# Optimization experiments

Measured on AMD Instinct MI355X. Metric: run time of the kernel, lower is better.

Reference implementation:

```python
import jax, jax.numpy as jnp
import numpy as np

TOKEN_BITS = 10
CODEBOOK_SIZE = 2 ** TOKEN_BITS
COMMITMENT_COST = 0.25
ENT_WEIGHT = 0.1
ENT_TEMP = 0.01
ENT_GAMMA = 1.0
EPS = 1e-5


def _make_codebook():
    bits_to_indices = 2 ** np.arange(TOKEN_BITS, dtype=np.int64)  # [c]
    all_codes = np.arange(CODEBOOK_SIZE, dtype=np.int64)  # [n]
    bits = ((all_codes[:, None] & bits_to_indices) != 0).astype(np.float32)
    return jnp.asarray(bits * 2.0 - 1.0)  # [n, c] in {-1, +1}


def setup_inputs() -> dict:
    key = jax.random.key(0)
    z = jax.random.normal(key, (64, 10, 32, 32), dtype=jnp.float32)  # [b, c, h, w]
    codebook = _make_codebook()  # [1024, 10]
    return {"z": z, "codebook": codebook}


def reference(z, codebook):
    # b c h w -> b h w c
    zc = jnp.transpose(z, (0, 2, 3, 1))
    # strategy == 'default': sign quantization to {-1, +1}
    z_hard = jnp.where(zc > 0.0, 1.0, -1.0).astype(zc.dtype)

    # bit-pack indices (bits represented by sign)
    bits_to_indices = (2 ** jnp.arange(TOKEN_BITS, dtype=jnp.int32))  # [c]
    min_encoding_indices = jnp.sum((zc > 0.0).astype(jnp.int32) * bits_to_indices, axis=-1)  # [b, h, w]

    # entropy loss (ent_strategy == 'default', training mode)
    d = -2.0 * jnp.einsum('bhwc,nc->bhwn', zc, codebook)
    affinity = (-d).reshape(-1, CODEBOOK_SIZE) / ENT_TEMP  # [bhw, n]
    probs = jax.nn.softmax(affinity, axis=-1)
    log_probs = jax.nn.log_softmax(affinity + EPS, axis=-1)
    per_sample_entropy = -jnp.mean(jnp.sum(probs * log_probs, axis=-1))
    avg_probs = jnp.mean(probs, axis=0)  # [n]
    avg_entropy = -jnp.sum(avg_probs * jnp.log(avg_probs + EPS)) * ENT_GAMMA
    entropy_loss = ENT_WEIGHT * (per_sample_entropy - avg_entropy)

    # straight-through estimator
    z_q = zc + jax.lax.stop_gradient(z_hard - zc)
    commitment_loss = COMMITMENT_COST * jnp.mean((jax.lax.stop_gradient(z_q) - zc) ** 2)
    loss = commitment_loss + entropy_loss

    z_q_out = jnp.transpose(z_q, (0, 3, 1, 2))  # b h w c -> b c h w
    return (z_q_out, loss, commitment_loss, entropy_loss,
            per_sample_entropy, avg_entropy, min_encoding_indices)
```

## Files before the change

kernel.cpp:

```cpp
#include <hip/hip_runtime.h>
#include <math.h>

#define NPIX   65536
#define NELEM  655360
#define NCODE  1024
#define CSTRIDE 1024
#define BSTRIDE 10240

#define SOFT_T 0.22f


__global__ void __launch_bounds__(256)
k_pixel(const float* __restrict__ z,
        float* __restrict__ zq,
        float* __restrict__ out_idx,
        float* __restrict__ ws) {
    __shared__ float hist[NCODE];
    __shared__ float s_av[256 * 11];
    __shared__ unsigned char s_ch[256 * 11];
    __shared__ float red[256];

    int tid = threadIdx.x;
    for (int i = tid; i < NCODE; i += 256) hist[i] = 0.f;
    __syncthreads();

    int p = blockIdx.x * 256 + tid;
    int b = p >> 10;
    int hw = p & 1023;
    const float* zp = z + b * BSTRIDE + hw;
    float*       qp = zq + b * BSTRIDE + hw;

    float* av = &s_av[tid * 11];
    unsigned char* ch = &s_ch[tid * 11];

    int idx = 0, k = 0;
    float commit = 0.f;
#pragma unroll
    for (int c = 0; c < 10; ++c) {
        float x = zp[c * CSTRIDE];
        float h = (x > 0.f) ? 1.f : -1.f;
        qp[c * CSTRIDE] = h;
        float d = h - x;
        commit = fmaf(d, d, commit);
        if (x > 0.f) idx |= (1 << c);
        float a = fabsf(x);
        if (a < SOFT_T) { av[k] = a; ch[k] = (unsigned char)c; ++k; }
    }
    out_idx[p] = (float)idx;

    int nsub = 1 << k;

    float Z = 1.f, U = 0.f, s = 0.f;
    int gray = 0;
    for (int m = 1; m < nsub; ++m) {
        int bit = __ffs(m) - 1;
        int bm = 1 << bit;
        gray ^= bm;
        float a = av[bit];
        s += (gray & bm) ? a : -a;
        float t = -400.f * s;
        float e = __expf(t);
        Z += e;
        U = fmaf(e, t, U);
    }
    float invZ = 1.f / Z;
    float plogp = U * invZ - logf(Z);

    atomicAdd(&hist[idx], invZ);
    gray = 0; s = 0.f;
    int cmask = 0;
    for (int m = 1; m < nsub; ++m) {
        int bit = __ffs(m) - 1;
        int bm = 1 << bit;
        gray ^= bm;
        cmask ^= (1 << ch[bit]);
        float a = av[bit];
        s += (gray & bm) ? a : -a;
        float e = __expf(-400.f * s);
        atomicAdd(&hist[idx ^ cmask], e * invZ);
    }

    red[tid] = plogp;
    __syncthreads();
    for (int st = 128; st > 0; st >>= 1) {
        if (tid < st) red[tid] += red[tid + st];
        __syncthreads();
    }
    if (tid == 0) atomicAdd(&ws[1], red[0]);
    __syncthreads();
    red[tid] = commit;
    __syncthreads();
    for (int st = 128; st > 0; st >>= 1) {
        if (tid < st) red[tid] += red[tid + st];
        __syncthreads();
    }
    if (tid == 0) atomicAdd(&ws[0], red[0]);

    __syncthreads();
    for (int i = tid; i < NCODE; i += 256)
        if (hist[i] != 0.f) atomicAdd(&ws[2 + i], hist[i]);
}

__global__ void k_final(const float* __restrict__ ws, float* __restrict__ out) {
    __shared__ float red[1024];
    int t = threadIdx.x;
    float a = ws[2 + t] * (1.f / 65536.f);
    red[t] = -a * logf(a + 1e-5f);
    __syncthreads();
    for (int s = 512; s > 0; s >>= 1) {
        if (t < s) red[t] += red[t + s];
        __syncthreads();
    }
    if (t == 0) {
        float avg_entropy = red[0];
        float pse = -ws[1] * (1.f / 65536.f);
        float commit = 0.25f * ws[0] * (1.f / (float)NELEM);
        float ent_loss = 0.1f * (pse - avg_entropy);
        out[NELEM + 0] = commit + ent_loss;
        out[NELEM + 1] = commit;
        out[NELEM + 2] = ent_loss;
        out[NELEM + 3] = pse;
        out[NELEM + 4] = avg_entropy;
    }
}

extern "C" void kernel_launch(void* const* d_in, const int* in_sizes, int n_in,
                              void* d_out, int out_size, void* d_ws, size_t ws_size,
                              hipStream_t stream) {
    const float* z = (const float*)d_in[0];
    float* out = (float*)d_out;
    float* ws = (float*)d_ws;

    hipMemsetAsync(ws, 0, (2 + NCODE) * sizeof(float), stream);
    k_pixel<<<NPIX / 256, 256, 0, stream>>>(z, out, out + NELEM + 5, ws);
    k_final<<<1, 1024, 0, stream>>>(ws, out);
}
```

Before: 82.30 us.

## Split each pixel's soft-code enumeration across four threads and fuse the final reduction

```diff
diff --git a/kernel.cpp b/kernel.cpp
--- a/kernel.cpp
+++ b/kernel.cpp
@@ -6,6 +6,7 @@
 #define NCODE  1024
 #define CSTRIDE 1024
 #define BSTRIDE 10240
+#define NBLK   1024
 
 #define SOFT_T 0.22f
 
@@ -14,20 +15,24 @@
 k_pixel(const float* __restrict__ z,
         float* __restrict__ zq,
         float* __restrict__ out_idx,
+        float* __restrict__ out_sc,
         float* __restrict__ ws) {
     __shared__ float hist[NCODE];
     __shared__ float s_av[256 * 11];
     __shared__ unsigned char s_ch[256 * 11];
     __shared__ float red[256];
+    __shared__ int s_last;
 
     int tid = threadIdx.x;
     for (int i = tid; i < NCODE; i += 256) hist[i] = 0.f;
     __syncthreads();
 
-    int p = blockIdx.x * 256 + tid;
+    int gt  = blockIdx.x * 256 + tid;
+    int p   = gt >> 2;
+    int sub = gt & 3;
     int b = p >> 10;
     int hw = p & 1023;
-    const float* zp = z + b * BSTRIDE + hw;
+    const float* zp = z  + b * BSTRIDE + hw;
     float*       qp = zq + b * BSTRIDE + hw;
 
     float* av = &s_av[tid * 11];
@@ -35,52 +40,69 @@
 
     int idx = 0, k = 0;
     float commit = 0.f;
+    float v[10];
 #pragma unroll
     for (int c = 0; c < 10; ++c) {
         float x = zp[c * CSTRIDE];
+        v[c] = x;
         float h = (x > 0.f) ? 1.f : -1.f;
-        qp[c * CSTRIDE] = h;
         float d = h - x;
         commit = fmaf(d, d, commit);
         if (x > 0.f) idx |= (1 << c);
         float a = fabsf(x);
         if (a < SOFT_T) { av[k] = a; ch[k] = (unsigned char)c; ++k; }
     }
-    out_idx[p] = (float)idx;
+#pragma unroll
+    for (int c = 0; c < 10; ++c)
+        if ((c & 3) == sub) qp[c * CSTRIDE] = (v[c] > 0.f) ? 1.f : -1.f;
+    if (sub == 0) out_idx[p] = (float)idx;
 
-    int nsub = 1 << k;
+    int kl = (k > 2) ? (k - 2) : 0;
+    int nIter = 1 << kl;
+    bool active = sub < (1 << (k < 2 ? k : 2));
+    float s0 = 0.f; int cm0 = 0;
+    if (k >= 1 && (sub & 1)) { s0 += av[k - 1]; cm0 |= 1 << ch[k - 1]; }
+    if (k >= 2 && (sub & 2)) { s0 += av[k - 2]; cm0 |= 1 << ch[k - 2]; }
 
-    float Z = 1.f, U = 0.f, s = 0.f;
-    int gray = 0;
-    for (int m = 1; m < nsub; ++m) {
-        int bit = __ffs(m) - 1;
-        int bm = 1 << bit;
-        gray ^= bm;
-        float a = av[bit];
-        s += (gray & bm) ? a : -a;
-        float t = -400.f * s;
-        float e = __expf(t);
-        Z += e;
-        U = fmaf(e, t, U);
+    float Z = 0.f, U = 0.f;
+    if (active) {
+        float t0 = -400.f * s0;
+        float e0 = __expf(t0);
+        Z = e0; U = e0 * t0;
+        int gray = 0; float s = s0;
+        for (int m = 1; m < nIter; ++m) {
+            int bit = __ffs(m) - 1;
+            int bm = 1 << bit;
+            gray ^= bm;
+            float a = av[bit];
+            s += (gray & bm) ? a : -a;
+            float t = -400.f * s;
+            float e = __expf(t);
+            Z += e;
+            U = fmaf(e, t, U);
+        }
     }
+    Z += __shfl_xor(Z, 1); Z += __shfl_xor(Z, 2);
+    U += __shfl_xor(U, 1); U += __shfl_xor(U, 2);
     float invZ = 1.f / Z;
     float plogp = U * invZ - logf(Z);
 
-    atomicAdd(&hist[idx], invZ);
-    gray = 0; s = 0.f;
-    int cmask = 0;
-    for (int m = 1; m < nsub; ++m) {
-        int bit = __ffs(m) - 1;
-        int bm = 1 << bit;
-        gray ^= bm;
-        cmask ^= (1 << ch[bit]);
-        float a = av[bit];
-        s += (gray & bm) ? a : -a;
-        float e = __expf(-400.f * s);
-        atomicAdd(&hist[idx ^ cmask], e * invZ);
+    if (active) {
+        atomicAdd(&hist[idx ^ cm0], __expf(-400.f * s0) * invZ);
+        int gray = 0, cmask = cm0; float s = s0;
+        for (int m = 1; m < nIter; ++m) {
+            int bit = __ffs(m) - 1;
+            int bm = 1 << bit;
+            gray ^= bm;
+            cmask ^= 1 << ch[bit];
+            float a = av[bit];
+            s += (gray & bm) ? a : -a;
+            float e = __expf(-400.f * s);
+            atomicAdd(&hist[idx ^ cmask], e * invZ);
+        }
     }
 
-    red[tid] = plogp;
+    red[tid] = (sub == 0) ? plogp : 0.f;
     __syncthreads();
     for (int st = 128; st > 0; st >>= 1) {
         if (tid < st) red[tid] += red[tid + st];
@@ -88,7 +110,7 @@
     }
     if (tid == 0) atomicAdd(&ws[1], red[0]);
     __syncthreads();
-    red[tid] = commit;
+    red[tid] = (sub == 0) ? commit : 0.f;
     __syncthreads();
     for (int st = 128; st > 0; st >>= 1) {
         if (tid < st) red[tid] += red[tid + st];
@@ -99,28 +121,36 @@
     __syncthreads();
     for (int i = tid; i < NCODE; i += 256)
         if (hist[i] != 0.f) atomicAdd(&ws[2 + i], hist[i]);
-}
 
-__global__ void k_final(const float* __restrict__ ws, float* __restrict__ out) {
-    __shared__ float red[1024];
-    int t = threadIdx.x;
-    float a = ws[2 + t] * (1.f / 65536.f);
-    red[t] = -a * logf(a + 1e-5f);
+    __threadfence();
+    if (tid == 0) {
+        unsigned done = atomicAdd((unsigned*)&ws[1026], 1u);
+        s_last = (done == NBLK - 1);
+    }
     __syncthreads();
-    for (int s = 512; s > 0; s >>= 1) {
-        if (t < s) red[t] += red[t + s];
+    if (s_last) {
+        float acc = 0.f;
+        for (int i = tid; i < NCODE; i += 256) {
+            float a = atomicAdd(&ws[2 + i], 0.f) * (1.f / 65536.f);
+            acc -= a * logf(a + 1e-5f);
+        }
+        red[tid] = acc;
         __syncthreads();
-    }
-    if (t == 0) {
-        float avg_entropy = red[0];
-        float pse = -ws[1] * (1.f / 65536.f);
-        float commit = 0.25f * ws[0] * (1.f / (float)NELEM);
-        float ent_loss = 0.1f * (pse - avg_entropy);
-        out[NELEM + 0] = commit + ent_loss;
-        out[NELEM + 1] = commit;
-        out[NELEM + 2] = ent_loss;
-        out[NELEM + 3] = pse;
-        out[NELEM + 4] = avg_entropy;
+        for (int st = 128; st > 0; st >>= 1) {
+            if (tid < st) red[tid] += red[tid + st];
+            __syncthreads();
+        }
+        if (tid == 0) {
+            float avg_entropy = red[0];
+            float pse = -atomicAdd(&ws[1], 0.f) * (1.f / 65536.f);
+            float cl  = 0.25f * atomicAdd(&ws[0], 0.f) * (1.f / (float)NELEM);
+            float ent_loss = 0.1f * (pse - avg_entropy);
+            out_sc[0] = cl + ent_loss;
+            out_sc[1] = cl;
+            out_sc[2] = ent_loss;
+            out_sc[3] = pse;
+            out_sc[4] = avg_entropy;
+        }
     }
 }
 
@@ -131,7 +161,6 @@
     float* out = (float*)d_out;
     float* ws = (float*)d_ws;
 
-    hipMemsetAsync(ws, 0, (2 + NCODE) * sizeof(float), stream);
-    k_pixel<<<NPIX / 256, 256, 0, stream>>>(z, out, out + NELEM + 5, ws);
-    k_final<<<1, 1024, 0, stream>>>(ws, out);
+    hipMemsetAsync(ws, 0, (2 + NCODE + 1) * sizeof(float), stream);
+    k_pixel<<<NBLK, 256, 0, stream>>>(z, out, out + NELEM + 5, out + NELEM, ws);
 }
```

Result: slower. 154.0 us (+87.2%).
